# Kernel tuning notes

Measured on AMD Instinct MI355X. Metric: run time of the kernel, lower is better.

Reference implementation:

```python
import math
import itertools
import jax, jax.numpy as jnp
import numpy as np

SEQ_LEN = 16
D_IN = 2048
TSS = 3          # temporal_set_size
D_OUT = 1128
PE_SCALE = 0.1
N_SUPPORT = 5
N_QUERIES = 1
LN_EPS = 1e-5


def _pos_enc(seq_len, d_model):
    pos = np.arange(seq_len, dtype=np.float32)[:, None]
    div = np.exp(np.arange(0, d_model, 2, dtype=np.float32) * -(math.log(10000.0) / d_model))
    pe = np.zeros((seq_len, d_model), dtype=np.float32)
    pe[:, 0::2] = np.sin(pos * div) * PE_SCALE
    pe[:, 1::2] = np.cos(pos * div) * PE_SCALE
    return jnp.asarray(pe)


def _tuples(seq_len, k):
    return np.asarray(list(itertools.combinations(range(seq_len), k)), dtype=np.int32)  # [T, k]


def setup_inputs() -> dict:
    key = jax.random.key(0)
    ks = jax.random.split(key, 8)
    return {
        "support_set": jax.random.normal(ks[0], (N_SUPPORT, SEQ_LEN, D_IN), jnp.float32),
        "queries": jax.random.normal(ks[1], (N_QUERIES, SEQ_LEN, D_IN), jnp.float32),
        "support_labels": jnp.arange(N_SUPPORT, dtype=jnp.int64),
        "wk": jax.random.normal(ks[2], (D_OUT, D_IN * TSS), jnp.float32) * 0.02,
        "bk": jax.random.normal(ks[3], (D_OUT,), jnp.float32) * 0.02,
        "wv": jax.random.normal(ks[4], (D_OUT, D_IN * TSS), jnp.float32) * 0.02,
        "bv": jax.random.normal(ks[5], (D_OUT,), jnp.float32) * 0.02,
        "gamma": jnp.ones((D_OUT,), jnp.float32),
        "beta": jnp.zeros((D_OUT,), jnp.float32),
    }


def _layer_norm(x, gamma, beta):
    mu = jnp.mean(x, axis=-1, keepdims=True)
    var = jnp.mean(jnp.square(x - mu), axis=-1, keepdims=True)
    return (x - mu) * jax.lax.rsqrt(var + LN_EPS) * gamma + beta


def reference(support_set, queries, support_labels, wk, bk, wv, bv, gamma, beta):
    tup = _tuples(SEQ_LEN, TSS)                      # [T, 3] static
    T = tup.shape[0]                                 # tuples_len = C(16,3) = 560
    pe = _pos_enc(SEQ_LEN, D_IN)                     # [S, D_IN]

    s = support_set + pe                             # [5, S, D_IN]
    q = queries + pe                                 # [1, S, D_IN]

    # gather frame tuples and flatten: [n, T, 3*D_IN]
    s_t = s[:, tup, :].reshape(N_SUPPORT, T, TSS * D_IN)
    q_t = q[:, tup, :].reshape(N_QUERIES, T, TSS * D_IN)

    s_ks = _layer_norm(s_t @ wk.T + bk, gamma, beta)  # [5, T, D_OUT]
    q_ks = _layer_norm(q_t @ wk.T + bk, gamma, beta)  # [1, T, D_OUT]
    s_vs = s_t @ wv.T + bv                            # [5, T, D_OUT]
    q_vs = q_t @ wv.T + bv                            # [1, T, D_OUT]

    # _extract_class_indices returns the label value itself -> direct row gather
    ck = s_ks[support_labels]                         # [C, T, D_OUT]
    cv = s_vs[support_labels]                         # [C, T, D_OUT]

    scores = jnp.einsum('qtd,csd->cqts', q_ks, ck) / math.sqrt(D_OUT)  # [C, Q, T, T]
    attn = jax.nn.softmax(scores, axis=-1)            # softmax over support tuples
    proto = jnp.einsum('cqts,csd->cqtd', attn, cv)    # [C, Q, T, D_OUT]

    diff = q_vs[None] - proto                         # [C, Q, T, D_OUT]
    dist = -jnp.sum(diff * diff, axis=(-2, -1)) / T   # [C, Q]
    logits = dist.T                                   # [Q, C]
    return logits
```

## Files before the change

kernel.cpp:

```cpp
#include <hip/hip_runtime.h>
#include <hip/hip_bf16.h>

#define SEQ 16
#define DIN 2048
#define TSS 3
#define DOUT 1128
#define DPAD 1152
#define NT 560
#define NTPAD 576
#define NSEQ 6
#define NCOL 6768

typedef __attribute__((ext_vector_type(4))) float f32x4;
typedef __attribute__((ext_vector_type(8))) short bf16x8;

__device__ __forceinline__ float bf2f(unsigned short h) {
    union { unsigned int u; float f; } c; c.u = ((unsigned int)h) << 16; return c.f;
}
__device__ __forceinline__ unsigned short f2bf(float f) {
    union { float f; unsigned int u; } c; c.f = f;
    unsigned int lsb = (c.u >> 16) & 1;
    c.u += 0x7fffu + lsb;
    return (unsigned short)(c.u >> 16);
}
__device__ __forceinline__ float loadf(const void* p, size_t i, int f32m) {
    return f32m ? ((const float*)p)[i] : bf2f(((const unsigned short*)p)[i]);
}
__device__ __forceinline__ int probe_f32(const void* gamma) {
    return (((const unsigned int*)gamma)[0] == 0x3F800000u) ? 1 : 0;
}
__device__ __forceinline__ int probe_i64(const void* labels) {
    return (((const long long*)labels)[1] == 1LL) ? 1 : 0;
}
__device__ __forceinline__ int get_label(const void* p, int c, int is64) {
    long long v = is64 ? ((const long long*)p)[c] : (long long)((const int*)p)[c];
    if (v < 0) v = 0; if (v > 4) v = 4;
    return (int)v;
}


__global__ __launch_bounds__(256) void k_build_x(
        const void* __restrict__ sup, const void* __restrict__ qry,
        const void* __restrict__ gamma,
        unsigned short* __restrict__ XF) {
    int f32m = probe_f32(gamma);
    int c8 = blockIdx.x * 256 + threadIdx.x;
    int idx512 = c8 >> 6;
    int rowgrp = idx512 >> 6, kt = idx512 & 63;
    int sub = c8 & 63;
    int r15 = sub & 15;
    int row = rowgrp * 16 + r15;
    int f = row & 15, n = row >> 4;
    int k = kt * 32 + (sub >> 4) * 8;
    bf16x8 ov;
#pragma unroll
    for (int j = 0; j < 8; ++j) {
        int d = k + j;
        float v = (n < 5) ? loadf(sup, (size_t)row * DIN + d, f32m)
                          : loadf(qry, (size_t)f * DIN + d, f32m);
        int m2 = d & ~1;
        float div = __expf(-(float)m2 * (9.210340371976184f / 2048.0f));
        float ang = (float)f * div;
        float pe = ((d & 1) ? __cosf(ang) : __sinf(ang)) * 0.1f;
        ov[j] = (short)f2bf(v + pe);
    }
    *(bf16x8*)(XF + (size_t)c8 * 8) = ov;
}

__global__ __launch_bounds__(256) void k_proj(
        const unsigned short* __restrict__ XF,
        const void* __restrict__ wk, const void* __restrict__ wv,
        const void* __restrict__ gamma,
        unsigned short* __restrict__ Pb) {
    int f32m = probe_f32(gamma);
    int cg = blockIdx.x;
    int tid = threadIdx.x;
    int w = tid >> 6, lane = tid & 63;
    int c16 = lane & 15, quad = lane >> 4;
    int col = cg * 16 + c16;
    int which = col / 3384; int rem = col - which * 3384;
    int seg = rem / DOUT;   int o = rem - seg * DOUT;
    const void* src = which ? wv : wk;
    size_t sbase = (size_t)o * (TSS * DIN) + (size_t)seg * DIN + (size_t)quad * 8;
    const unsigned short* aF = XF + lane * 8;

    f32x4 acc[6];
#pragma unroll
    for (int m = 0; m < 6; ++m) acc[m] = (f32x4){0.f, 0.f, 0.f, 0.f};

    int ktb = w * 16;
    if (f32m) {
        const float* s32 = (const float*)src + sbase;
#pragma unroll 2
        for (int kt = ktb; kt < ktb + 16; ++kt) {
            f32x4 w0 = *(const f32x4*)(s32 + (size_t)kt * 32);
            f32x4 w1 = *(const f32x4*)(s32 + (size_t)kt * 32 + 4);
            bf16x8 b;
#pragma unroll
            for (int j = 0; j < 4; ++j) {
                b[j]     = (short)f2bf(w0[j]);
                b[4 + j] = (short)f2bf(w1[j]);
            }
#pragma unroll
            for (int m = 0; m < 6; ++m) {
                bf16x8 a = *(const bf16x8*)(aF + ((size_t)(m * 64 + kt) << 9));
                acc[m] = __builtin_amdgcn_mfma_f32_16x16x32_bf16(a, b, acc[m], 0, 0, 0);
            }
        }
    } else {
        const unsigned short* s16 = (const unsigned short*)src + sbase;
#pragma unroll 2
        for (int kt = ktb; kt < ktb + 16; ++kt) {
            bf16x8 b = *(const bf16x8*)(s16 + (size_t)kt * 32);
#pragma unroll
            for (int m = 0; m < 6; ++m) {
                bf16x8 a = *(const bf16x8*)(aF + ((size_t)(m * 64 + kt) << 9));
                acc[m] = __builtin_amdgcn_mfma_f32_16x16x32_bf16(a, b, acc[m], 0, 0, 0);
            }
        }
    }

    __shared__ float red[3 * 6 * 64 * 4];
    if (w > 0) {
#pragma unroll
        for (int m = 0; m < 6; ++m)
#pragma unroll
            for (int r = 0; r < 4; ++r)
                red[(((w - 1) * 6 + m) * 64 + lane) * 4 + r] = acc[m][r];
    }
    __syncthreads();
    if (w == 0) {
#pragma unroll
        for (int m = 0; m < 6; ++m) {
#pragma unroll
            for (int r = 0; r < 4; ++r) {
                float s = acc[m][r]
                        + red[((0 * 6 + m) * 64 + lane) * 4 + r]
                        + red[((1 * 6 + m) * 64 + lane) * 4 + r]
                        + red[((2 * 6 + m) * 64 + lane) * 4 + r];
                int row = m * 16 + quad * 4 + r;
                Pb[(size_t)row * NCOL + col] = f2bf(s);
            }
        }
    }
}

__global__ __launch_bounds__(256) void k_combine_ln(
        const unsigned short* __restrict__ Pb,
        const void* __restrict__ bk, const void* __restrict__ bv,
        const void* __restrict__ gamma, const void* __restrict__ beta,
        unsigned short* __restrict__ ksF, unsigned short* __restrict__ vs) {
    int n = blockIdx.x / NT, t = blockIdx.x % NT;
    int f32m = probe_f32(gamma);
    int idx = t, fi, fj, fk;
    for (fi = 0;; ++fi) { int c2 = (15 - fi) * (14 - fi) / 2; if (idx < c2) break; idx -= c2; }
    for (fj = fi + 1;; ++fj) { int c1 = 15 - fj; if (idx < c1) break; idx -= c1; }
    fk = fj + 1 + idx;
    size_t ri = (size_t)(n * 16 + fi) * NCOL;
    size_t rj = (size_t)(n * 16 + fj) * NCOL;
    size_t rk = (size_t)(n * 16 + fk) * NCOL;

    float kv[5], vv[5];
    float s = 0.f, s2 = 0.f;
#pragma unroll
    for (int it = 0; it < 5; ++it) {
        int o = threadIdx.x + it * 256;
        kv[it] = 0.f; vv[it] = 0.f;
        if (o < DOUT) {
            float a = bf2f(Pb[ri + o]) + bf2f(Pb[rj + DOUT + o])
                    + bf2f(Pb[rk + 2 * DOUT + o]) + loadf(bk, o, f32m);
            float b = bf2f(Pb[ri + 3 * DOUT + o]) + bf2f(Pb[rj + 4 * DOUT + o])
                    + bf2f(Pb[rk + 5 * DOUT + o]) + loadf(bv, o, f32m);
            kv[it] = a; vv[it] = b;
            s += a; s2 += a * a;
        }
    }
    __shared__ float red[8];
#pragma unroll
    for (int off = 32; off; off >>= 1) { s += __shfl_down(s, off); s2 += __shfl_down(s2, off); }
    int wid = threadIdx.x >> 6;
    if ((threadIdx.x & 63) == 0) { red[wid] = s; red[4 + wid] = s2; }
    __syncthreads();
    s = red[0] + red[1] + red[2] + red[3];
    s2 = red[4] + red[5] + red[6] + red[7];
    float mu = s / (float)DOUT;
    float var = s2 / (float)DOUT - mu * mu;
    float rstd = rsqrtf(var + 1e-5f);

    size_t ntbase = ((size_t)(n * 36 + (t >> 4)) * 36) * 512 + (size_t)(t & 15) * 8;
    size_t vbase = ((size_t)n * NT + t) * DPAD;
#pragma unroll
    for (int it = 0; it < 5; ++it) {
        int o = threadIdx.x + it * 256;
        if (o < DPAD) {
            float kres = 0.f;
            if (o < DOUT)
                kres = (kv[it] - mu) * rstd * loadf(gamma, o, f32m) + loadf(beta, o, f32m);
            ksF[ntbase + ((size_t)(o >> 5) << 9) + (((o >> 3) & 3) << 7) + (o & 7)] =
                (o < DOUT) ? f2bf(kres) : 0;
            vs[vbase + o] = (o < DOUT) ? f2bf(vv[it]) : 0;
        }
    }
}

__global__ __launch_bounds__(256) void k_transpose(
        const unsigned short* __restrict__ vs, unsigned short* __restrict__ vsTF) {
    int b = blockIdx.x;
    int tt = b % 18; b /= 18; int ot = b % 36; int n = b / 36;
    int t0 = tt * 32, o0 = ot * 32;
    int tx = threadIdx.x & 31, ty = threadIdx.x >> 5;
    __shared__ unsigned short tile[32][33];
#pragma unroll
    for (int i = 0; i < 4; ++i) {
        int t = t0 + ty + 8 * i;
        tile[ty + 8 * i][tx] = (t < NT) ? vs[((size_t)n * NT + t) * DPAD + o0 + tx] : 0;
    }
    __syncthreads();
#pragma unroll
    for (int i = 0; i < 4; ++i) {
        int r = ty + 8 * i;
        size_t addr = ((size_t)(n * 72 + ot * 2 + (r >> 4)) * 18 + tt) * 512
                    + (size_t)((tx >> 3) * 16 + (r & 15)) * 8 + (tx & 7);
        vsTF[addr] = tile[tx][r];
    }
}

__global__ __launch_bounds__(256) void k_scores(
        const unsigned short* __restrict__ ksF, const void* __restrict__ labels,
        float* __restrict__ scores) {
    int b = blockIdx.x;
    int c = b % 5; int rest = b / 5;
    int tm = rest / 9, tn = rest % 9;
    int tid = threadIdx.x;
    int w = tid >> 6, lane = tid & 63;
    int c16 = lane & 15, quad = lane >> 4;
    int lab = get_label(labels, c, probe_i64(labels));
    const unsigned short* aF[4];
    const unsigned short* bF[4];
#pragma unroll
    for (int i = 0; i < 4; ++i) {
        aF[i] = ksF + (((size_t)(5 * 36 + tm * 4 + i) * 36) << 9) + lane * 8;
        bF[i] = ksF + (((size_t)(lab * 36 + tn * 4 + i) * 36) << 9) + lane * 8;
    }
    f32x4 acc[4][4];
#pragma unroll
    for (int i = 0; i < 4; ++i)
#pragma unroll
        for (int j = 0; j < 4; ++j) acc[i][j] = (f32x4){0.f, 0.f, 0.f, 0.f};

    int ktb = w * 9;
#pragma unroll 2
    for (int kt = ktb; kt < ktb + 9; ++kt) {
        bf16x8 a[4], bv4[4];
#pragma unroll
        for (int i = 0; i < 4; ++i) a[i]   = *(const bf16x8*)(aF[i] + ((size_t)kt << 9));
#pragma unroll
        for (int j = 0; j < 4; ++j) bv4[j] = *(const bf16x8*)(bF[j] + ((size_t)kt << 9));
#pragma unroll
        for (int i = 0; i < 4; ++i)
#pragma unroll
            for (int j = 0; j < 4; ++j)
                acc[i][j] = __builtin_amdgcn_mfma_f32_16x16x32_bf16(a[i], bv4[j], acc[i][j], 0, 0, 0);
    }
    __shared__ float red[3 * 16 * 64 * 4];
    if (w > 0) {
#pragma unroll
        for (int i = 0; i < 4; ++i)
#pragma unroll
            for (int j = 0; j < 4; ++j)
#pragma unroll
                for (int r = 0; r < 4; ++r)
                    red[(((w - 1) * 16 + i * 4 + j) * 64 + lane) * 4 + r] = acc[i][j][r];
    }
    __syncthreads();
    if (w == 0) {
        const float scale = 0.029774540f;
#pragma unroll
        for (int i = 0; i < 4; ++i)
#pragma unroll
            for (int j = 0; j < 4; ++j) {
                int t = i * 4 + j;
#pragma unroll
                for (int r = 0; r < 4; ++r) {
                    float s = acc[i][j][r]
                            + red[((0 * 16 + t) * 64 + lane) * 4 + r]
                            + red[((1 * 16 + t) * 64 + lane) * 4 + r]
                            + red[((2 * 16 + t) * 64 + lane) * 4 + r];
                    int tq = tm * 64 + i * 16 + quad * 4 + r;
                    int ts = tn * 64 + j * 16 + c16;
                    scores[((size_t)c * NTPAD + tq) * NTPAD + ts] = s * scale;
                }
            }
    }
}

__global__ __launch_bounds__(256) void k_softmax(
        const float* __restrict__ scores, unsigned short* __restrict__ attnF) {
    int row = blockIdx.x * 4 + (threadIdx.x >> 6);
    int lane = threadIdx.x & 63;
    int c = row / NTPAD, tq = row % NTPAD;
    unsigned short* dstc = attnF + ((size_t)(c * 36 + (tq >> 4)) * 18) * 512 + (size_t)(tq & 15) * 8;
    if (tq >= NT) {
#pragma unroll
        for (int i = 0; i < 9; ++i) {
            int ts = lane + i * 64;
            dstc[((ts >> 5) << 9) + ((ts >> 3) & 3) * 128 + (ts & 7)] = 0;
        }
        return;
    }
    const float* src = scores + (size_t)row * NTPAD;
    float vals[9];
    float m = -1e30f;
#pragma unroll
    for (int i = 0; i < 9; ++i) {
        int idx = lane + i * 64;
        vals[i] = (idx < NT) ? src[idx] : -1e30f;
        m = fmaxf(m, vals[i]);
    }
#pragma unroll
    for (int off = 32; off; off >>= 1) m = fmaxf(m, __shfl_xor(m, off));
    float s = 0.f;
#pragma unroll
    for (int i = 0; i < 9; ++i) {
        int idx = lane + i * 64;
        vals[i] = (idx < NT) ? __expf(vals[i] - m) : 0.f;
        s += vals[i];
    }
#pragma unroll
    for (int off = 32; off; off >>= 1) s += __shfl_xor(s, off);
    float inv = 1.f / s;
#pragma unroll
    for (int i = 0; i < 9; ++i) {
        int ts = lane + i * 64;
        dstc[((ts >> 5) << 9) + ((ts >> 3) & 3) * 128 + (ts & 7)] =
            (ts < NT) ? f2bf(vals[i] * inv) : 0;
    }
}

__global__ __launch_bounds__(128) void k_proto_dist(
        const unsigned short* __restrict__ attnF, const unsigned short* __restrict__ vs,
        const unsigned short* __restrict__ vsTF,
        const void* __restrict__ labels, float* __restrict__ parts) {
    int b = blockIdx.x;
    int c = b / 162; int rest = b % 162;
    int tm = rest / 18, tn = rest % 18;
    int tid = threadIdx.x;
    int w = tid >> 6, lane = tid & 63;
    int c16 = lane & 15, quad = lane >> 4;
    int lab = get_label(labels, c, probe_i64(labels));
    const unsigned short* aF = attnF + ((size_t)(c * 36 + tm * 4) * 18) * 512 + lane * 8;
    const unsigned short* bF = vsTF + ((size_t)(lab * 72 + tn * 4) * 18) * 512 + lane * 8;
    f32x4 acc[4][4];
#pragma unroll
    for (int i = 0; i < 4; ++i)
#pragma unroll
        for (int j = 0; j < 4; ++j) acc[i][j] = (f32x4){0.f, 0.f, 0.f, 0.f};

    int ktb = w * 9;
#pragma unroll 2
    for (int kt = ktb; kt < ktb + 9; ++kt) {
        bf16x8 a[4], bv4[4];
#pragma unroll
        for (int i = 0; i < 4; ++i) a[i]   = *(const bf16x8*)(aF + ((size_t)(i * 18 + kt) << 9));
#pragma unroll
        for (int j = 0; j < 4; ++j) bv4[j] = *(const bf16x8*)(bF + ((size_t)(j * 18 + kt) << 9));
#pragma unroll
        for (int i = 0; i < 4; ++i)
#pragma unroll
            for (int j = 0; j < 4; ++j)
                acc[i][j] = __builtin_amdgcn_mfma_f32_16x16x32_bf16(a[i], bv4[j], acc[i][j], 0, 0, 0);
    }
    __shared__ float red[16 * 64 * 4];
    if (w == 1) {
#pragma unroll
        for (int i = 0; i < 4; ++i)
#pragma unroll
            for (int j = 0; j < 4; ++j)
#pragma unroll
                for (int r = 0; r < 4; ++r)
                    red[((i * 4 + j) * 64 + lane) * 4 + r] = acc[i][j][r];
    }
    __syncthreads();
    if (w == 0) {
        const unsigned short* qv = vs + (size_t)5 * NT * DPAD;
        float part = 0.f;
#pragma unroll
        for (int i = 0; i < 4; ++i)
#pragma unroll
            for (int j = 0; j < 4; ++j) {
                int t = i * 4 + j;
#pragma unroll
                for (int r = 0; r < 4; ++r) {
                    float s = acc[i][j][r] + red[(t * 64 + lane) * 4 + r];
                    int tq = tm * 64 + i * 16 + quad * 4 + r;
                    int o  = tn * 64 + j * 16 + c16;
                    if (tq < NT && o < DOUT) {
                        float d = bf2f(qv[(size_t)tq * DPAD + o]) - s;
                        part += d * d;
                    }
                }
            }
#pragma unroll
        for (int off = 32; off; off >>= 1) part += __shfl_down(part, off);
        if (lane == 0) parts[blockIdx.x] = part;
    }
}

__global__ __launch_bounds__(320) void k_final(const float* __restrict__ parts,
                                               const void* __restrict__ gamma,
                                               void* __restrict__ out) {
    int c = threadIdx.x >> 6;
    int lane = threadIdx.x & 63;
    float s = 0.f;
    for (int i = lane; i < 162; i += 64) s += parts[c * 162 + i];
#pragma unroll
    for (int off = 32; off; off >>= 1) s += __shfl_down(s, off);
    if (lane == 0) {
        float v = -s * (1.0f / (float)NT);
        if (probe_f32(gamma)) ((float*)out)[c] = v;
        else ((unsigned short*)out)[c] = f2bf(v);
    }
}

extern "C" void kernel_launch(void* const* d_in, const int* in_sizes, int n_in,
                              void* d_out, int out_size, void* d_ws, size_t ws_size,
                              hipStream_t stream) {
    const void* sup   = d_in[0];
    const void* qry   = d_in[1];
    const void* labs  = d_in[2];
    const void* wk    = d_in[3];
    const void* bk    = d_in[4];
    const void* wv    = d_in[5];
    const void* bv    = d_in[6];
    const void* gamma = d_in[7];
    const void* beta  = d_in[8];

    char* ws = (char*)d_ws;
    unsigned short* XF     = (unsigned short*)(ws + 256);
    unsigned short* Pb     = (unsigned short*)(ws + 393472);
    float*          parts  = (float*)(ws + 2992384);
    unsigned short* ksF    = (unsigned short*)(ws + 33326080);
    unsigned short* vsb    = (unsigned short*)(ws + 41288704);
    float*          scores = (float*)(ws + 49030144);
    unsigned short* attnF  = (unsigned short*)(ws + 55665664);
    unsigned short* vsTF   = (unsigned short*)(ws + 58983424);

    k_build_x   <<<96, 256, 0, stream>>>(sup, qry, gamma, XF);
    k_proj      <<<423, 256, 0, stream>>>(XF, wk, wv, gamma, Pb);
    k_combine_ln<<<NSEQ * NT, 256, 0, stream>>>(Pb, bk, bv, gamma, beta, ksF, vsb);
    k_transpose <<<5 * 36 * 18, 256, 0, stream>>>(vsb, vsTF);
    k_scores    <<<405, 256, 0, stream>>>(ksF, labs, scores);
    k_softmax   <<<720, 256, 0, stream>>>(scores, attnF);
    k_proto_dist<<<810, 128, 0, stream>>>(attnF, vsb, vsTF, labs, parts);
    k_final     <<<1, 320, 0, stream>>>(parts, gamma, d_out);
}
```

Measured before the change: 185.9 us.

## Fuse V transpose into combine-LN and spread split-K reductions across waves

The combine/LayerNorm kernel now handles 8 tuples per block with one wave per tuple. It stages the support V rows in shared memory and writes the transposed fragment layout directly, so the separate transpose kernel and the round trip of support V through global memory go away. The split-K epilogues in the scores and proto-dist kernels are rebalanced so every wave reduces and writes its own slice instead of wave 0 doing all of it. The cost is a larger per-thread register array (18 values each for K and V) and more shared-memory traffic in the reductions.

```diff
diff --git a/kernel.cpp b/kernel.cpp
--- a/kernel.cpp
+++ b/kernel.cpp
@@ -149,79 +149,86 @@
         const unsigned short* __restrict__ Pb,
         const void* __restrict__ bk, const void* __restrict__ bv,
         const void* __restrict__ gamma, const void* __restrict__ beta,
-        unsigned short* __restrict__ ksF, unsigned short* __restrict__ vs) {
-    int n = blockIdx.x / NT, t = blockIdx.x % NT;
+        unsigned short* __restrict__ ksF, unsigned short* __restrict__ vs,
+        unsigned short* __restrict__ vsTF) {
+    int n = blockIdx.x / 70;
+    int tg = blockIdx.x % 70;
     int f32m = probe_f32(gamma);
-    int idx = t, fi, fj, fk;
-    for (fi = 0;; ++fi) { int c2 = (15 - fi) * (14 - fi) / 2; if (idx < c2) break; idx -= c2; }
-    for (fj = fi + 1;; ++fj) { int c1 = 15 - fj; if (idx < c1) break; idx -= c1; }
-    fk = fj + 1 + idx;
-    size_t ri = (size_t)(n * 16 + fi) * NCOL;
-    size_t rj = (size_t)(n * 16 + fj) * NCOL;
-    size_t rk = (size_t)(n * 16 + fk) * NCOL;
-
-    float kv[5], vv[5];
-    float s = 0.f, s2 = 0.f;
-#pragma unroll
-    for (int it = 0; it < 5; ++it) {
-        int o = threadIdx.x + it * 256;
-        kv[it] = 0.f; vv[it] = 0.f;
-        if (o < DOUT) {
-            float a = bf2f(Pb[ri + o]) + bf2f(Pb[rj + DOUT + o])
-                    + bf2f(Pb[rk + 2 * DOUT + o]) + loadf(bk, o, f32m);
-            float b = bf2f(Pb[ri + 3 * DOUT + o]) + bf2f(Pb[rj + 4 * DOUT + o])
-                    + bf2f(Pb[rk + 5 * DOUT + o]) + loadf(bv, o, f32m);
-            kv[it] = a; vv[it] = b;
-            s += a; s2 += a * a;
-        }
-    }
-    __shared__ float red[8];
-#pragma unroll
-    for (int off = 32; off; off >>= 1) { s += __shfl_down(s, off); s2 += __shfl_down(s2, off); }
-    int wid = threadIdx.x >> 6;
-    if ((threadIdx.x & 63) == 0) { red[wid] = s; red[4 + wid] = s2; }
-    __syncthreads();
-    s = red[0] + red[1] + red[2] + red[3];
-    s2 = red[4] + red[5] + red[6] + red[7];
-    float mu = s / (float)DOUT;
-    float var = s2 / (float)DOUT - mu * mu;
-    float rstd = rsqrtf(var + 1e-5f);
-
-    size_t ntbase = ((size_t)(n * 36 + (t >> 4)) * 36) * 512 + (size_t)(t & 15) * 8;
-    size_t vbase = ((size_t)n * NT + t) * DPAD;
-#pragma unroll
-    for (int it = 0; it < 5; ++it) {
-        int o = threadIdx.x + it * 256;
-        if (o < DPAD) {
+    int lane = threadIdx.x & 63, w = threadIdx.x >> 6;
+    __shared__ unsigned short vtile[8][1152];
+
+    for (int b = 0; b < 2; ++b) {
+        int tl = w + 4 * b;
+        int t = tg * 8 + tl;
+        int idx = t, fi, fj, fk;
+        for (fi = 0;; ++fi) { int c2 = (15 - fi) * (14 - fi) / 2; if (idx < c2) break; idx -= c2; }
+        for (fj = fi + 1;; ++fj) { int c1 = 15 - fj; if (idx < c1) break; idx -= c1; }
+        fk = fj + 1 + idx;
+        size_t ri = (size_t)(n * 16 + fi) * NCOL;
+        size_t rj = (size_t)(n * 16 + fj) * NCOL;
+        size_t rk = (size_t)(n * 16 + fk) * NCOL;
+
+        float kv[18], vv[18];
+        float s = 0.f, s2 = 0.f;
+#pragma unroll
+        for (int i = 0; i < 18; ++i) {
+            int o = lane + i * 64;
+            kv[i] = 0.f; vv[i] = 0.f;
+            if (o < DOUT) {
+                float a = bf2f(Pb[ri + o]) + bf2f(Pb[rj + DOUT + o])
+                        + bf2f(Pb[rk + 2 * DOUT + o]) + loadf(bk, o, f32m);
+                float bb = bf2f(Pb[ri + 3 * DOUT + o]) + bf2f(Pb[rj + 4 * DOUT + o])
+                         + bf2f(Pb[rk + 5 * DOUT + o]) + loadf(bv, o, f32m);
+                kv[i] = a; vv[i] = bb;
+                s += a; s2 += a * a;
+            }
+        }
+#pragma unroll
+        for (int off = 32; off; off >>= 1) { s += __shfl_down(s, off); s2 += __shfl_down(s2, off); }
+        s = __shfl(s, 0); s2 = __shfl(s2, 0);
+        float mu = s / (float)DOUT;
+        float var = s2 / (float)DOUT - mu * mu;
+        float rstd = rsqrtf(var + 1e-5f);
+
+        size_t ntbase = ((size_t)(n * 36 + (t >> 4)) * 36) * 512 + (size_t)(t & 15) * 8;
+#pragma unroll
+        for (int i = 0; i < 18; ++i) {
+            int o = lane + i * 64;
             float kres = 0.f;
             if (o < DOUT)
-                kres = (kv[it] - mu) * rstd * loadf(gamma, o, f32m) + loadf(beta, o, f32m);
+                kres = (kv[i] - mu) * rstd * loadf(gamma, o, f32m) + loadf(beta, o, f32m);
             ksF[ntbase + ((size_t)(o >> 5) << 9) + (((o >> 3) & 3) << 7) + (o & 7)] =
                 (o < DOUT) ? f2bf(kres) : 0;
-            vs[vbase + o] = (o < DOUT) ? f2bf(vv[it]) : 0;
-        }
-    }
-}
-
-__global__ __launch_bounds__(256) void k_transpose(
-        const unsigned short* __restrict__ vs, unsigned short* __restrict__ vsTF) {
-    int b = blockIdx.x;
-    int tt = b % 18; b /= 18; int ot = b % 36; int n = b / 36;
-    int t0 = tt * 32, o0 = ot * 32;
-    int tx = threadIdx.x & 31, ty = threadIdx.x >> 5;
-    __shared__ unsigned short tile[32][33];
-#pragma unroll
-    for (int i = 0; i < 4; ++i) {
-        int t = t0 + ty + 8 * i;
-        tile[ty + 8 * i][tx] = (t < NT) ? vs[((size_t)n * NT + t) * DPAD + o0 + tx] : 0;
+            unsigned short vb = (o < DOUT) ? f2bf(vv[i]) : 0;
+            if (n == 5) {
+                if (o < DOUT) vs[(size_t)(5 * NT + t) * DPAD + o] = vb;
+            } else {
+                vtile[tl][o] = vb;
+            }
+        }
     }
     __syncthreads();
-#pragma unroll
-    for (int i = 0; i < 4; ++i) {
-        int r = ty + 8 * i;
-        size_t addr = ((size_t)(n * 72 + ot * 2 + (r >> 4)) * 18 + tt) * 512
-                    + (size_t)((tx >> 3) * 16 + (r & 15)) * 8 + (tx & 7);
-        vsTF[addr] = tile[tx][r];
+    if (n < 5) {
+        int tt = tg >> 2;
+        int q  = tg & 3;
+        for (int c = threadIdx.x; c < 1152; c += 256) {
+            int o = c;
+            union { unsigned short u[8]; bf16x8 v; } pk;
+#pragma unroll
+            for (int e = 0; e < 8; ++e) pk.u[e] = vtile[e][o];
+            size_t addr = ((size_t)(n * 72 + (o >> 4)) * 18 + tt) * 512
+                        + (size_t)(q * 16 + (o & 15)) * 8;
+            *(bf16x8*)(vsTF + addr) = pk.v;
+        }
+        if (tg == 69) {
+            bf16x8 z = (bf16x8){0, 0, 0, 0, 0, 0, 0, 0};
+            for (int c = threadIdx.x; c < 2304; c += 256) {
+                int qq = 2 + (c / 1152); int o = c % 1152;
+                size_t addr = ((size_t)(n * 72 + (o >> 4)) * 18 + 17) * 512
+                            + (size_t)(qq * 16 + (o & 15)) * 8;
+                *(bf16x8*)(vsTF + addr) = z;
+            }
+        }
     }
 }
 
@@ -262,35 +269,40 @@
             for (int j = 0; j < 4; ++j)
                 acc[i][j] = __builtin_amdgcn_mfma_f32_16x16x32_bf16(a[i], bv4[j], acc[i][j], 0, 0, 0);
     }
-    __shared__ float red[3 * 16 * 64 * 4];
-    if (w > 0) {
-#pragma unroll
-        for (int i = 0; i < 4; ++i)
+    __shared__ float red[16 * 3 * 64 * 4];
+#pragma unroll
+    for (int i = 0; i < 4; ++i) {
+        if (i != w) {
+            int slot = (w < i) ? w : w - 1;
 #pragma unroll
             for (int j = 0; j < 4; ++j)
 #pragma unroll
                 for (int r = 0; r < 4; ++r)
-                    red[(((w - 1) * 16 + i * 4 + j) * 64 + lane) * 4 + r] = acc[i][j][r];
+                    red[(((i * 4 + j) * 3 + slot) * 64 + lane) * 4 + r] = acc[i][j][r];
+        }
     }
     __syncthreads();
-    if (w == 0) {
+    {
         const float scale = 0.029774540f;
-#pragma unroll
-        for (int i = 0; i < 4; ++i)
-#pragma unroll
-            for (int j = 0; j < 4; ++j) {
-                int t = i * 4 + j;
-#pragma unroll
-                for (int r = 0; r < 4; ++r) {
-                    float s = acc[i][j][r]
-                            + red[((0 * 16 + t) * 64 + lane) * 4 + r]
-                            + red[((1 * 16 + t) * 64 + lane) * 4 + r]
-                            + red[((2 * 16 + t) * 64 + lane) * 4 + r];
-                    int tq = tm * 64 + i * 16 + quad * 4 + r;
-                    int ts = tn * 64 + j * 16 + c16;
-                    scores[((size_t)c * NTPAD + tq) * NTPAD + ts] = s * scale;
-                }
-            }
+        f32x4 own[4];
+        if (w == 0)      { own[0]=acc[0][0]; own[1]=acc[0][1]; own[2]=acc[0][2]; own[3]=acc[0][3]; }
+        else if (w == 1) { own[0]=acc[1][0]; own[1]=acc[1][1]; own[2]=acc[1][2]; own[3]=acc[1][3]; }
+        else if (w == 2) { own[0]=acc[2][0]; own[1]=acc[2][1]; own[2]=acc[2][2]; own[3]=acc[2][3]; }
+        else             { own[0]=acc[3][0]; own[1]=acc[3][1]; own[2]=acc[3][2]; own[3]=acc[3][3]; }
+#pragma unroll
+        for (int j = 0; j < 4; ++j) {
+            int t = w * 4 + j;
+#pragma unroll
+            for (int r = 0; r < 4; ++r) {
+                float s = own[j][r]
+                        + red[((t * 3 + 0) * 64 + lane) * 4 + r]
+                        + red[((t * 3 + 1) * 64 + lane) * 4 + r]
+                        + red[((t * 3 + 2) * 64 + lane) * 4 + r];
+                int tq = tm * 64 + w * 16 + quad * 4 + r;
+                int ts = tn * 64 + j * 16 + c16;
+                scores[((size_t)c * NTPAD + tq) * NTPAD + ts] = s * scale;
+            }
+        }
     }
 }
 
@@ -371,38 +383,61 @@
                 acc[i][j] = __builtin_amdgcn_mfma_f32_16x16x32_bf16(a[i], bv4[j], acc[i][j], 0, 0, 0);
     }
     __shared__ float red[16 * 64 * 4];
-    if (w == 1) {
-#pragma unroll
-        for (int i = 0; i < 4; ++i)
+    if (w == 0) {
+#pragma unroll
+        for (int i = 2; i < 4; ++i)
 #pragma unroll
             for (int j = 0; j < 4; ++j)
 #pragma unroll
                 for (int r = 0; r < 4; ++r)
                     red[((i * 4 + j) * 64 + lane) * 4 + r] = acc[i][j][r];
+    } else {
+#pragma unroll
+        for (int i = 0; i < 2; ++i)
+#pragma unroll
+            for (int j = 0; j < 4; ++j)
+#pragma unroll
+                for (int r = 0; r < 4; ++r)
+                    red[((i * 4 + j) * 64 + lane) * 4 + r] = acc[i][j][r];
     }
     __syncthreads();
-    if (w == 0) {
+    {
         const unsigned short* qv = vs + (size_t)5 * NT * DPAD;
         float part = 0.f;
-#pragma unroll
-        for (int i = 0; i < 4; ++i)
-#pragma unroll
-            for (int j = 0; j < 4; ++j) {
-                int t = i * 4 + j;
-#pragma unroll
-                for (int r = 0; r < 4; ++r) {
-                    float s = acc[i][j][r] + red[(t * 64 + lane) * 4 + r];
-                    int tq = tm * 64 + i * 16 + quad * 4 + r;
-                    int o  = tn * 64 + j * 16 + c16;
-                    if (tq < NT && o < DOUT) {
-                        float d = bf2f(qv[(size_t)tq * DPAD + o]) - s;
-                        part += d * d;
+        if (w == 0) {
+#pragma unroll
+            for (int i = 0; i < 2; ++i)
+#pragma unroll
+                for (int j = 0; j < 4; ++j)
+#pragma unroll
+                    for (int r = 0; r < 4; ++r) {
+                        float s = acc[i][j][r] + red[((i * 4 + j) * 64 + lane) * 4 + r];
+                        int tq = tm * 64 + i * 16 + quad * 4 + r;
+                        int o  = tn * 64 + j * 16 + c16;
+                        if (tq < NT && o < DOUT) {
+                            float d = bf2f(qv[(size_t)tq * DPAD + o]) - s;
+                            part += d * d;
+                        }
                     }
-                }
-            }
+        } else {
+#pragma unroll
+            for (int i = 2; i < 4; ++i)
+#pragma unroll
+                for (int j = 0; j < 4; ++j)
+#pragma unroll
+                    for (int r = 0; r < 4; ++r) {
+                        float s = acc[i][j][r] + red[((i * 4 + j) * 64 + lane) * 4 + r];
+                        int tq = tm * 64 + i * 16 + quad * 4 + r;
+                        int o  = tn * 64 + j * 16 + c16;
+                        if (tq < NT && o < DOUT) {
+                            float d = bf2f(qv[(size_t)tq * DPAD + o]) - s;
+                            part += d * d;
+                        }
+                    }
+        }
 #pragma unroll
         for (int off = 32; off; off >>= 1) part += __shfl_down(part, off);
-        if (lane == 0) parts[blockIdx.x] = part;
+        if (lane == 0) parts[blockIdx.x * 2 + w] = part;
     }
 }
 
@@ -412,7 +447,7 @@
     int c = threadIdx.x >> 6;
     int lane = threadIdx.x & 63;
     float s = 0.f;
-    for (int i = lane; i < 162; i += 64) s += parts[c * 162 + i];
+    for (int i = lane; i < 324; i += 64) s += parts[c * 324 + i];
 #pragma unroll
     for (int off = 32; off; off >>= 1) s += __shfl_down(s, off);
     if (lane == 0) {
@@ -447,8 +482,7 @@
 
     k_build_x   <<<96, 256, 0, stream>>>(sup, qry, gamma, XF);
     k_proj      <<<423, 256, 0, stream>>>(XF, wk, wv, gamma, Pb);
-    k_combine_ln<<<NSEQ * NT, 256, 0, stream>>>(Pb, bk, bv, gamma, beta, ksF, vsb);
-    k_transpose <<<5 * 36 * 18, 256, 0, stream>>>(vsb, vsTF);
+    k_combine_ln<<<NSEQ * 70, 256, 0, stream>>>(Pb, bk, bv, gamma, beta, ksF, vsb, vsTF);
     k_scores    <<<405, 256, 0, stream>>>(ksF, labs, scores);
     k_softmax   <<<720, 256, 0, stream>>>(scores, attnF);
     k_proto_dist<<<810, 128, 0, stream>>>(attnF, vsb, vsTF, labs, parts);
```

Measured after the change: 194.9 us. 4.9% more time.
